# Kernel tuning notes

Hardware: AMD Instinct MI355X
Metric: run time of the kernel (lower is better)

Reference implementation:

```python
import jax, jax.numpy as jnp
import numpy as np

DOWNSAMPLE = 1  # downsample_factor


def _grid(out_h, out_w):
    # rows: x in [-1,1] along width, y in [-1,1] along height, ones
    x_t = jnp.linspace(-1.0, 1.0, out_w, dtype=jnp.float32)
    y_t = jnp.linspace(-1.0, 1.0, out_h, dtype=jnp.float32)
    xg = jnp.tile(x_t[None, :], (out_h, 1)).reshape(-1)
    yg = jnp.tile(y_t[:, None], (1, out_w)).reshape(-1)
    return jnp.stack([xg, yg, jnp.ones_like(xg)], axis=0)  # [3, P]


def spatial_transform(X, theta):
    B, C, H, W = X.shape
    out_h, out_w = H // DOWNSAMPLE, W // DOWNSAMPLE
    grid = _grid(out_h, out_w)                               # [3, P]
    Tg = jnp.einsum('bij,jp->bip', theta.reshape(B, 2, 3), grid)  # [B,2,P]
    x_s, y_s = Tg[:, 0], Tg[:, 1]                            # [B, P]

    # map from [-1,1] to pixel coords (same convention as original)
    x = (x_s + 1.0) * (W / 2.0)
    y = (y_s + 1.0) * (H / 2.0)
    x0 = jnp.floor(x).astype(jnp.int32)
    x1 = x0 + 1
    y0 = jnp.floor(y).astype(jnp.int32)
    y1 = y0 + 1
    x0c = jnp.clip(x0, 0, W - 1)
    x1c = jnp.clip(x1, 0, W - 1)
    y0c = jnp.clip(y0, 0, H - 1)
    y1c = jnp.clip(y1, 0, H - 1)

    im = jnp.transpose(X, (0, 2, 3, 1)).reshape(B, H * W, C)  # [B, HW, C]

    def gather(yi, xi):
        idx = yi * W + xi                                      # [B, P]
        return jnp.take_along_axis(im, idx[:, :, None], axis=1)  # [B, P, C]

    Ia = gather(y0c, x0c)
    Ib = gather(y1c, x0c)
    Ic = gather(y0c, x1c)
    Id = gather(y1c, x1c)

    x0f = x0c.astype(jnp.float32)
    x1f = x1c.astype(jnp.float32)
    y0f = y0c.astype(jnp.float32)
    y1f = y1c.astype(jnp.float32)
    wa = ((x1f - x) * (y1f - y))[:, :, None]
    wb = ((x1f - x) * (y - y0f))[:, :, None]
    wc = ((x - x0f) * (y1f - y))[:, :, None]
    wd = ((x - x0f) * (y - y0f))[:, :, None]

    out = wa * Ia + wb * Ib + wc * Ic + wd * Id               # [B, P, C]
    out = out.reshape(B, out_h, out_w, C)
    return jnp.transpose(out, (0, 3, 1, 2))                   # NCHW


def setup_inputs() -> dict:
    key = jax.random.key(0)
    kx, kt = jax.random.split(key)
    X = jax.random.normal(kx, (32, 3, 512, 512), dtype=jnp.float32)
    # theta near identity + noise for sensible transforms
    ident = jnp.array([1.0, 0.0, 0.0, 0.0, 1.0, 0.0], dtype=jnp.float32)
    theta = ident[None, :] + 0.1 * jax.random.normal(kt, (32, 6), dtype=jnp.float32)
    return {"X": X, "theta": theta}


def reference(X, theta):
    return spatial_transform(X, theta)
```

## Files before the change

kernel.cpp:

```cpp
#include <hip/hip_runtime.h>


#define ST_H 512
#define ST_W 512
#define ST_C 3
#define ST_HW (ST_H * ST_W)

typedef float f2 __attribute__((ext_vector_type(2)));
typedef float f4 __attribute__((ext_vector_type(4)));
struct __attribute__((packed, aligned(4))) f2_a4 { f2 v; };

__global__ __launch_bounds__(256) void st_bilinear_kernel(
    const float* __restrict__ X,
    const float* __restrict__ theta,
    float* __restrict__ out,
    int chunk)
{
    __shared__ float sb[ST_C * 16 * 64];

    int bid = blockIdx.x;
    bid = (bid & 7) * chunk + (bid >> 3);

    const int b   = bid >> 8;
    const int idx = bid & 255;
    const int tx  = idx & 7;
    const int ty  = idx >> 3;
    const int hb  = ty << 4;

    const int tid  = (int)threadIdx.x;
    const int lane = tid & 63;
    const int r    = tid >> 6;
    const int w    = (tx << 6) + lane;

    const float* t = theta + b * 6;
    const float t00 = t[0], t01 = t[1], t02 = t[2];
    const float t10 = t[3], t11 = t[4], t12 = t[5];

    const float STEP = (float)(2.0 / 511.0);
    const float xg  = fmaf((float)w, STEP, -1.0f);
    const float xb0 = fmaf(t00, xg, t02);
    const float yb0 = fmaf(t10, xg, t12);

    const float* __restrict__ Xb = X + (size_t)b * (ST_C * ST_HW);

#pragma unroll
    for (int k = 0; k < 4; ++k) {
        const int row = r + (k << 2);
        const int h = hb + row;
        const float yg = fmaf((float)h, STEP, -1.0f);
        const float x = (fmaf(t01, yg, xb0) + 1.0f) * 256.0f;
        const float y = (fmaf(t11, yg, yb0) + 1.0f) * 256.0f;

        const int x0 = (int)floorf(x);
        const int y0 = (int)floorf(y);

        const int x0c = min(max(x0, 0), ST_W - 1);
        const int x1c = min(max(x0 + 1, 0), ST_W - 1);
        const int y0c = min(max(y0, 0), ST_H - 1);
        const int y1c = min(max(y0 + 1, 0), ST_H - 1);

        const float x0f = (float)x0c, x1f = (float)x1c;
        const float y0f = (float)y0c, y1f = (float)y1c;
        const float wa = (x1f - x) * (y1f - y);
        const float wb = (x1f - x) * (y - y0f);
        const float wc = (x - x0f) * (y1f - y);
        const float wd = (x - x0f) * (y - y0f);

        const int xa = min(max(x0, 0), ST_W - 2);
        const bool hi = (x0 >= ST_W - 1);
        const bool lo = (x0 < 0);

        const int ia = y0c * ST_W + xa;
        const int ib = y1c * ST_W + xa;

#pragma unroll
        for (int c = 0; c < ST_C; ++c) {
            const float* __restrict__ Xc = Xb + c * ST_HW;
            const f2 p = ((const f2_a4*)(Xc + ia))->v;
            const f2 q = ((const f2_a4*)(Xc + ib))->v;
            const float Ia = hi ? p.y : p.x;
            const float Ic = lo ? p.x : p.y;
            const float Ib = hi ? q.y : q.x;
            const float Id = lo ? q.x : q.y;
            sb[(c * 16 + row) * 64 + lane] =
                wa * Ia + wb * Ib + wc * Ic + wd * Id;
        }
    }

    __syncthreads();

    float* __restrict__ ob = out + (size_t)b * (ST_C * ST_HW);
#pragma unroll
    for (int k = 0; k < 3; ++k) {
        const int f = (k * 256 + tid) * 4;
        const int c = f >> 10;
        const int rem = f & 1023;
        const int row = rem >> 6;
        const int col = rem & 63;
        const f4 v = *(const f4*)&sb[f];
        __builtin_nontemporal_store(
            v, (f4*)(ob + c * ST_HW + (hb + row) * ST_W + (tx << 6) + col));
    }
}

extern "C" void kernel_launch(void* const* d_in, const int* in_sizes, int n_in,
                              void* d_out, int out_size, void* d_ws, size_t ws_size,
                              hipStream_t stream) {
    const float* X     = (const float*)d_in[0];
    const float* theta = (const float*)d_in[1];
    float* out         = (float*)d_out;

    const int B = in_sizes[1] / 6;
    const int block = 256;
    const int grid = B * 256;
    const int chunk = grid / 8;

    st_bilinear_kernel<<<grid, block, 0, stream>>>(X, theta, out, chunk);
}
```

Baseline: 40.97 us.

## Stage per-tile source footprint in LDS and sample from shared memory

Each block maps the four corners of its 64x16 output tile to find the bounding box of source pixels. When that box fits in a 32x88 LDS tile, the block loads it channel by channel with coalesced row loads and takes the bilinear taps from shared memory. Otherwise it falls back to direct global gathers. The old LDS transpose is dropped, so outputs go out as scalar nontemporal stores instead of float4. The change aims to turn scattered global gathers into coalesced loads, at the cost of extra barriers, clamping logic and narrower stores.

```diff
diff --git a/kernel.cpp b/kernel.cpp
--- a/kernel.cpp
+++ b/kernel.cpp
@@ -5,10 +5,25 @@
 #define ST_W 512
 #define ST_C 3
 #define ST_HW (ST_H * ST_W)
+#define RMAX 32
+#define PITCH 88
+#define HALFP 44
 
 typedef float f2 __attribute__((ext_vector_type(2)));
-typedef float f4 __attribute__((ext_vector_type(4)));
 struct __attribute__((packed, aligned(4))) f2_a4 { f2 v; };
+
+__device__ __forceinline__ void st_xy(float t00, float t01, float t02,
+                                      float t10, float t11, float t12,
+                                      int w, int h, float& x, float& y)
+{
+    const float STEP = (float)(2.0 / 511.0);
+    const float xg  = fmaf((float)w, STEP, -1.0f);
+    const float yg  = fmaf((float)h, STEP, -1.0f);
+    const float xb0 = fmaf(t00, xg, t02);
+    const float yb0 = fmaf(t10, xg, t12);
+    x = (fmaf(t01, yg, xb0) + 1.0f) * 256.0f;
+    y = (fmaf(t11, yg, yb0) + 1.0f) * 256.0f;
+}
 
 __global__ __launch_bounds__(256) void st_bilinear_kernel(
     const float* __restrict__ X,
@@ -16,7 +31,7 @@
     float* __restrict__ out,
     int chunk)
 {
-    __shared__ float sb[ST_C * 16 * 64];
+    __shared__ float sb[RMAX * PITCH];
 
     int bid = blockIdx.x;
     bid = (bid & 7) * chunk + (bid >> 3);
@@ -25,31 +40,46 @@
     const int idx = bid & 255;
     const int tx  = idx & 7;
     const int ty  = idx >> 3;
-    const int hb  = ty << 4;
+    const int w0t = tx << 6;
+    const int h0t = ty << 4;
 
     const int tid  = (int)threadIdx.x;
     const int lane = tid & 63;
-    const int r    = tid >> 6;
-    const int w    = (tx << 6) + lane;
+    const int wid  = tid >> 6;
+    const int w    = w0t + lane;
 
     const float* t = theta + b * 6;
     const float t00 = t[0], t01 = t[1], t02 = t[2];
     const float t10 = t[3], t11 = t[4], t12 = t[5];
 
-    const float STEP = (float)(2.0 / 511.0);
-    const float xg  = fmaf((float)w, STEP, -1.0f);
-    const float xb0 = fmaf(t00, xg, t02);
-    const float yb0 = fmaf(t10, xg, t12);
+    float xmin = 1e30f, xmax = -1e30f, ymin = 1e30f, ymax = -1e30f;
+#pragma unroll
+    for (int i = 0; i < 2; ++i)
+#pragma unroll
+        for (int j = 0; j < 2; ++j) {
+            float xx, yy;
+            st_xy(t00, t01, t02, t10, t11, t12,
+                  w0t + i * 63, h0t + j * 15, xx, yy);
+            xmin = fminf(xmin, xx); xmax = fmaxf(xmax, xx);
+            ymin = fminf(ymin, yy); ymax = fmaxf(ymax, yy);
+        }
+    const int xlo = (int)floorf(xmin) - 1;
+    const int ylo = (int)floorf(ymin) - 1;
+    const int RX  = (int)floorf(xmax) + 2 - xlo + 1;
+    const int RY  = (int)floorf(ymax) + 2 - ylo + 1;
+    const bool fast = (RX <= PITCH) && (RY <= RMAX);
 
-    const float* __restrict__ Xb = X + (size_t)b * (ST_C * ST_HW);
+    float wa[4], wb[4], wc[4], wd[4];
+    int soff[4];
+    int ia[4], ib[4];
+    bool hi[4], lo[4];
+    int opix[4];
 
 #pragma unroll
     for (int k = 0; k < 4; ++k) {
-        const int row = r + (k << 2);
-        const int h = hb + row;
-        const float yg = fmaf((float)h, STEP, -1.0f);
-        const float x = (fmaf(t01, yg, xb0) + 1.0f) * 256.0f;
-        const float y = (fmaf(t11, yg, yb0) + 1.0f) * 256.0f;
+        const int h = h0t + wid + (k << 2);
+        float x, y;
+        st_xy(t00, t01, t02, t10, t11, t12, w, h, x, y);
 
         const int x0 = (int)floorf(x);
         const int y0 = (int)floorf(y);
@@ -61,45 +91,72 @@
 
         const float x0f = (float)x0c, x1f = (float)x1c;
         const float y0f = (float)y0c, y1f = (float)y1c;
-        const float wa = (x1f - x) * (y1f - y);
-        const float wb = (x1f - x) * (y - y0f);
-        const float wc = (x - x0f) * (y1f - y);
-        const float wd = (x - x0f) * (y - y0f);
+        wa[k] = (x1f - x) * (y1f - y);
+        wb[k] = (x1f - x) * (y - y0f);
+        wc[k] = (x - x0f) * (y1f - y);
+        wd[k] = (x - x0f) * (y - y0f);
+
+        soff[k] = (y0 - ylo) * PITCH + (x0 - xlo);
 
         const int xa = min(max(x0, 0), ST_W - 2);
-        const bool hi = (x0 >= ST_W - 1);
-        const bool lo = (x0 < 0);
+        hi[k] = (x0 >= ST_W - 1);
+        lo[k] = (x0 < 0);
+        ia[k] = y0c * ST_W + xa;
+        ib[k] = y1c * ST_W + xa;
 
-        const int ia = y0c * ST_W + xa;
-        const int ib = y1c * ST_W + xa;
+        opix[k] = h * ST_W + w;
+    }
 
+    const float* __restrict__ Xb = X + (size_t)b * (ST_C * ST_HW);
+    float* __restrict__ ob = out + (size_t)b * (ST_C * ST_HW);
+
+    if (fast) {
 #pragma unroll
         for (int c = 0; c < ST_C; ++c) {
             const float* __restrict__ Xc = Xb + c * ST_HW;
-            const f2 p = ((const f2_a4*)(Xc + ia))->v;
-            const f2 q = ((const f2_a4*)(Xc + ib))->v;
-            const float Ia = hi ? p.y : p.x;
-            const float Ic = lo ? p.x : p.y;
-            const float Ib = hi ? q.y : q.x;
-            const float Id = lo ? q.x : q.y;
-            sb[(c * 16 + row) * 64 + lane] =
-                wa * Ia + wb * Ib + wc * Ic + wd * Id;
+            if (c) __syncthreads();
+#pragma unroll
+            for (int it = 0; it < RMAX / 4; ++it) {
+                const int row = wid + (it << 2);
+                if (row < RY) {
+                    const int grow = min(max(ylo + row, 0), ST_H - 1);
+                    const float* __restrict__ rp = Xc + (grow << 9);
+                    if (lane < HALFP) {
+                        const int c0 = min(max(xlo + 2 * lane,     0), ST_W - 1);
+                        const int c1 = min(max(xlo + 2 * lane + 1, 0), ST_W - 1);
+                        f2 v; v.x = rp[c0]; v.y = rp[c1];
+                        *(f2*)&sb[row * PITCH + 2 * lane] = v;
+                    }
+                }
+            }
+            __syncthreads();
+#pragma unroll
+            for (int k = 0; k < 4; ++k) {
+                const float* sp = &sb[soff[k]];
+                const float Ia = sp[0];
+                const float Ic = sp[1];
+                const float Ib = sp[PITCH];
+                const float Id = sp[PITCH + 1];
+                const float v = wa[k] * Ia + wb[k] * Ib + wc[k] * Ic + wd[k] * Id;
+                __builtin_nontemporal_store(v, ob + c * ST_HW + opix[k]);
+            }
         }
-    }
-
-    __syncthreads();
-
-    float* __restrict__ ob = out + (size_t)b * (ST_C * ST_HW);
+    } else {
 #pragma unroll
-    for (int k = 0; k < 3; ++k) {
-        const int f = (k * 256 + tid) * 4;
-        const int c = f >> 10;
-        const int rem = f & 1023;
-        const int row = rem >> 6;
-        const int col = rem & 63;
-        const f4 v = *(const f4*)&sb[f];
-        __builtin_nontemporal_store(
-            v, (f4*)(ob + c * ST_HW + (hb + row) * ST_W + (tx << 6) + col));
+        for (int k = 0; k < 4; ++k) {
+#pragma unroll
+            for (int c = 0; c < ST_C; ++c) {
+                const float* __restrict__ Xc = Xb + c * ST_HW;
+                const f2 p = ((const f2_a4*)(Xc + ia[k]))->v;
+                const f2 q = ((const f2_a4*)(Xc + ib[k]))->v;
+                const float Ia = hi[k] ? p.y : p.x;
+                const float Ic = lo[k] ? p.x : p.y;
+                const float Ib = hi[k] ? q.y : q.x;
+                const float Id = lo[k] ? q.x : q.y;
+                const float v = wa[k] * Ia + wb[k] * Ib + wc[k] * Ic + wd[k] * Id;
+                __builtin_nontemporal_store(v, ob + c * ST_HW + opix[k]);
+            }
+        }
     }
 }
 
```

Result: slower. 46.80 us (+14.2%).
